# Kernel optimization log

Measured on AMD Instinct MI355X. Metric: run time of the kernel, lower is better.

Reference implementation:

```python
import jax, jax.numpy as jnp
import numpy as np

B, D, H = 65536, 32, 128


def setup_inputs() -> dict:
    key = jax.random.key(0)
    ks = jax.random.split(key, 6)
    return {
        "x": jax.random.normal(ks[0], (B, 1, D), dtype=jnp.float32),
        "W1": jax.random.normal(ks[1], (D, H), dtype=jnp.float32) * (1.0 / np.sqrt(D)),
        "b1": jax.random.normal(ks[2], (H,), dtype=jnp.float32) * 0.01,
        "W2": jax.random.normal(ks[3], (H, D), dtype=jnp.float32) * (1.0 / np.sqrt(H)),
        "b2": jax.random.normal(ks[4], (D,), dtype=jnp.float32) * 0.01,
        "theta_0": jnp.array([0.5], dtype=jnp.float32),
    }


def reference(x, W1, b1, W2, b2, theta_0):
    # x: (B, 1, D). Network u: D -> H -> D with tanh (transformation=none, no bounds).
    xf = x[:, 0, :]  # (B, D)

    def u_fn(xv):  # (D,) -> (D,)
        h = jnp.tanh(xv @ W1 + b1)
        return h @ W2 + b2

    # div u = trace of per-sample Jacobian, computed in ONE vectorized forward-mode
    # sweep (replaces the per-dimension torch.autograd.grad loop).
    div_u = jax.vmap(lambda xv: jnp.trace(jax.jacfwd(u_fn)(xv)))(xf)  # (B,)

    u_x = jax.vmap(u_fn)(xf)  # (B, D)
    grad_log_pi = -xf  # standard normal: grad log pi(x) = -x, shape (B, D)
    grad_log_pi_u = jnp.sum(grad_log_pi * u_x, axis=-1)  # (B,)  == (B,1,D)@(B,D,1) flattened

    out = (grad_log_pi_u + div_u + theta_0)[:, None]  # (B, 1)
    return out
```

## Files before the change

### kernel.cpp

```cpp
#include <hip/hip_runtime.h>


#define NROWS 65536
#define DD 32
#define HH 128
#define NTILE 25

typedef __attribute__((ext_vector_type(8))) short short8;
typedef __attribute__((ext_vector_type(4))) float f32x4;

static __device__ __forceinline__ unsigned short f2bf(float f) {
    unsigned u = __float_as_uint(f);
    u += 0x7fff + ((u >> 16) & 1);
    return (unsigned short)(u >> 16);
}
static __device__ __forceinline__ float bf2f(unsigned short h) {
    return __uint_as_float(((unsigned)h) << 16);
}

__global__ __launch_bounds__(512, 4) void stein_fused(
    const float* __restrict__ x, const float* __restrict__ W1,
    const float* __restrict__ b1, const float* __restrict__ W2,
    const float* __restrict__ b2, const float* __restrict__ theta,
    float* __restrict__ out) {
    __shared__ unsigned short lb[NTILE * 512];
    __shared__ float cs[HH];
    __shared__ float b1s[HH];

    const int tid = threadIdx.x;
    const int lane = tid & 63;
    const int wv = tid >> 6;
    const int quad = lane >> 4;
    const int cl = lane & 15;
    const int rowbase = blockIdx.x * 128 + wv * 16;

    const float* xr = x + (size_t)(rowbase + cl) * DD + quad * 8;
    const float4 x0 = *(const float4*)xr;
    const float4 x1 = *(const float4*)(xr + 4);

    if (tid < 256) {
        const int n = tid & 127;
        const int half = tid >> 7;
        const int t = n >> 4, cc = n & 15;
#pragma unroll
        for (int g = 0; g < 2; ++g) {
            const int kg = half * 2 + g;
            short8 hi, lo;
#pragma unroll
            for (int j = 0; j < 8; ++j) {
                const float w = W1[(kg * 8 + j) * HH + n];
                const unsigned short h = f2bf(w);
                hi[j] = (short)h;
                lo[j] = (short)f2bf(w - bf2f(h));
            }
            *(short8*)(lb + t * 512 + (kg * 16 + cc) * 8) = hi;
            *(short8*)(lb + (8 + t) * 512 + (kg * 16 + cc) * 8) = lo;
        }
    } else if (tid < 384) {
        const int n = tid - 256;
        const int t2 = 16 + (n >> 4), cc = n & 15;
        float row[32];
        const float4* wr = (const float4*)(W2 + n * DD);
#pragma unroll
        for (int q = 0; q < 8; ++q) {
            const float4 f = wr[q];
            row[4 * q + 0] = f.x;
            row[4 * q + 1] = f.y;
            row[4 * q + 2] = f.z;
            row[4 * q + 3] = f.w;
        }
        float acc = 0.f;
#pragma unroll
        for (int k = 0; k < 32; ++k) acc = fmaf(W1[k * HH + n], row[k], acc);
        cs[n] = acc;
#pragma unroll
        for (int g = 0; g < 4; ++g) {
            short8 v;
#pragma unroll
            for (int j = 0; j < 8; ++j) v[j] = (short)f2bf(row[g * 8 + j]);
            *(short8*)(lb + t2 * 512 + (g * 16 + cc) * 8) = v;
        }
    } else {
        const int u = tid - 384;
        if (u < 16) {
#pragma unroll
            for (int g = 0; g < 4; ++g) {
                short8 v;
#pragma unroll
                for (int j = 0; j < 8; ++j)
                    v[j] = (u == 0) ? (short)f2bf(b2[g * 8 + j]) : (short)0;
                *(short8*)(lb + 24 * 512 + (g * 16 + u) * 8) = v;
            }
        }
        b1s[u] = b1[u];
    }
    __syncthreads();

    const float xv[8] = {x0.x, x0.y, x0.z, x0.w, x1.x, x1.y, x1.z, x1.w};
    short8 aHi, aLo;
#pragma unroll
    for (int j = 0; j < 8; ++j) {
        const unsigned short h = f2bf(xv[j]);
        aHi[j] = (short)h;
        aLo[j] = (short)f2bf(xv[j] - bf2f(h));
    }

    const f32x4 zero = {0.f, 0.f, 0.f, 0.f};
    float sa[4] = {0.f, 0.f, 0.f, 0.f};

#pragma unroll
    for (int t = 0; t < 8; ++t) {
        const short8 bH = *(const short8*)(lb + t * 512 + lane * 8);
        const short8 bL = *(const short8*)(lb + (8 + t) * 512 + lane * 8);
        const short8 bW = *(const short8*)(lb + (16 + t) * 512 + lane * 8);
        f32x4 z = zero;
        z = __builtin_amdgcn_mfma_f32_16x16x32_bf16(aLo, bH, z, 0, 0, 0);
        z = __builtin_amdgcn_mfma_f32_16x16x32_bf16(aHi, bL, z, 0, 0, 0);
        z = __builtin_amdgcn_mfma_f32_16x16x32_bf16(aHi, bH, z, 0, 0, 0);
        const f32x4 v = __builtin_amdgcn_mfma_f32_16x16x32_bf16(aHi, bW, zero, 0, 0, 0);
        const float ck = cs[t * 16 + cl];
        const float bb = b1s[t * 16 + cl];
#pragma unroll
        for (int r = 0; r < 4; ++r) {
            const float zz = z[r] + bb;
            const float e = __expf(2.f * zz);
            const float h = fmaf(-2.f, __builtin_amdgcn_rcpf(e + 1.f), 1.f);
            sa[r] += ck - h * fmaf(h, ck, v[r]);
        }
    }
    {
        const short8 bW = *(const short8*)(lb + 24 * 512 + lane * 8);
        const f32x4 v = __builtin_amdgcn_mfma_f32_16x16x32_bf16(aHi, bW, zero, 0, 0, 0);
#pragma unroll
        for (int r = 0; r < 4; ++r) sa[r] -= v[r];
    }

#pragma unroll
    for (int r = 0; r < 4; ++r) {
#pragma unroll
        for (int m = 1; m < 16; m <<= 1) sa[r] += __shfl_xor(sa[r], m, 64);
    }

    if (cl == 0) {
        const float th = theta[0];
        float4 o;
        o.x = sa[0] + th;
        o.y = sa[1] + th;
        o.z = sa[2] + th;
        o.w = sa[3] + th;
        *(float4*)(out + rowbase + quad * 4) = o;
    }
}

extern "C" void kernel_launch(void* const* d_in, const int* in_sizes, int n_in,
                              void* d_out, int out_size, void* d_ws, size_t ws_size,
                              hipStream_t stream) {
    const float* x = (const float*)d_in[0];
    const float* W1 = (const float*)d_in[1];
    const float* b1 = (const float*)d_in[2];
    const float* W2 = (const float*)d_in[3];
    const float* b2 = (const float*)d_in[4];
    const float* theta = (const float*)d_in[5];
    float* out = (float*)d_out;

    stein_fused<<<NROWS / 128, 512, 0, stream>>>(x, W1, b1, W2, b2, theta, out);
}
```

Baseline: 72.03 us.

## Process two 16-row tiles per wave to amortize weight setup across more rows

Each wave now handles 32 rows instead of 16, reusing the same LDS B-fragments for two sets of MFMAs. The block count halves, so the per-block weight conversion prologue is amortized over twice as many rows. The c_k dot product moves to the previously idle threads 384-511, and the c and b1 values are packed into one float2 LDS array. Launch bounds drop to 2 blocks per SM, trading occupancy for more instruction-level parallelism and extra registers.

```diff
diff --git a/kernel.cpp b/kernel.cpp
--- a/kernel.cpp
+++ b/kernel.cpp
@@ -18,25 +18,27 @@
     return __uint_as_float(((unsigned)h) << 16);
 }
 
-__global__ __launch_bounds__(512, 4) void stein_fused(
+__global__ __launch_bounds__(512, 2) void stein_fused(
     const float* __restrict__ x, const float* __restrict__ W1,
     const float* __restrict__ b1, const float* __restrict__ W2,
     const float* __restrict__ b2, const float* __restrict__ theta,
     float* __restrict__ out) {
     __shared__ unsigned short lb[NTILE * 512];
-    __shared__ float cs[HH];
-    __shared__ float b1s[HH];
+    __shared__ float2 cb[HH];
 
     const int tid = threadIdx.x;
     const int lane = tid & 63;
     const int wv = tid >> 6;
     const int quad = lane >> 4;
     const int cl = lane & 15;
-    const int rowbase = blockIdx.x * 128 + wv * 16;
+    const int rowbase = blockIdx.x * 256 + wv * 32;
 
-    const float* xr = x + (size_t)(rowbase + cl) * DD + quad * 8;
-    const float4 x0 = *(const float4*)xr;
-    const float4 x1 = *(const float4*)(xr + 4);
+    const float* xr0 = x + (size_t)(rowbase + cl) * DD + quad * 8;
+    const float* xr1 = x + (size_t)(rowbase + 16 + cl) * DD + quad * 8;
+    const float4 x00 = *(const float4*)xr0;
+    const float4 x01 = *(const float4*)(xr0 + 4);
+    const float4 x10 = *(const float4*)xr1;
+    const float4 x11 = *(const float4*)(xr1 + 4);
 
     if (tid < 256) {
         const int n = tid & 127;
@@ -59,29 +61,32 @@
     } else if (tid < 384) {
         const int n = tid - 256;
         const int t2 = 16 + (n >> 4), cc = n & 15;
-        float row[32];
         const float4* wr = (const float4*)(W2 + n * DD);
 #pragma unroll
-        for (int q = 0; q < 8; ++q) {
-            const float4 f = wr[q];
-            row[4 * q + 0] = f.x;
-            row[4 * q + 1] = f.y;
-            row[4 * q + 2] = f.z;
-            row[4 * q + 3] = f.w;
-        }
-        float acc = 0.f;
-#pragma unroll
-        for (int k = 0; k < 32; ++k) acc = fmaf(W1[k * HH + n], row[k], acc);
-        cs[n] = acc;
-#pragma unroll
         for (int g = 0; g < 4; ++g) {
+            const float4 f0 = wr[2 * g];
+            const float4 f1 = wr[2 * g + 1];
             short8 v;
-#pragma unroll
-            for (int j = 0; j < 8; ++j) v[j] = (short)f2bf(row[g * 8 + j]);
+            v[0] = (short)f2bf(f0.x); v[1] = (short)f2bf(f0.y);
+            v[2] = (short)f2bf(f0.z); v[3] = (short)f2bf(f0.w);
+            v[4] = (short)f2bf(f1.x); v[5] = (short)f2bf(f1.y);
+            v[6] = (short)f2bf(f1.z); v[7] = (short)f2bf(f1.w);
             *(short8*)(lb + t2 * 512 + (g * 16 + cc) * 8) = v;
         }
     } else {
         const int u = tid - 384;
+        float row[DD];
+        const float4* wr = (const float4*)(W2 + u * DD);
+#pragma unroll
+        for (int q = 0; q < 8; ++q) {
+            const float4 f = wr[q];
+            row[4 * q + 0] = f.x; row[4 * q + 1] = f.y;
+            row[4 * q + 2] = f.z; row[4 * q + 3] = f.w;
+        }
+        float acc = 0.f;
+#pragma unroll
+        for (int k = 0; k < DD; ++k) acc = fmaf(W1[k * HH + u], row[k], acc);
+        cb[u] = make_float2(acc, b1[u]);
         if (u < 16) {
 #pragma unroll
             for (int g = 0; g < 4; ++g) {
@@ -92,63 +97,85 @@
                 *(short8*)(lb + 24 * 512 + (g * 16 + u) * 8) = v;
             }
         }
-        b1s[u] = b1[u];
     }
     __syncthreads();
 
-    const float xv[8] = {x0.x, x0.y, x0.z, x0.w, x1.x, x1.y, x1.z, x1.w};
-    short8 aHi, aLo;
+    short8 aHi0, aLo0, aHi1, aLo1;
+    {
+        const float xv0[8] = {x00.x, x00.y, x00.z, x00.w, x01.x, x01.y, x01.z, x01.w};
+        const float xv1[8] = {x10.x, x10.y, x10.z, x10.w, x11.x, x11.y, x11.z, x11.w};
 #pragma unroll
-    for (int j = 0; j < 8; ++j) {
-        const unsigned short h = f2bf(xv[j]);
-        aHi[j] = (short)h;
-        aLo[j] = (short)f2bf(xv[j] - bf2f(h));
+        for (int j = 0; j < 8; ++j) {
+            unsigned short h0 = f2bf(xv0[j]);
+            aHi0[j] = (short)h0;
+            aLo0[j] = (short)f2bf(xv0[j] - bf2f(h0));
+            unsigned short h1 = f2bf(xv1[j]);
+            aHi1[j] = (short)h1;
+            aLo1[j] = (short)f2bf(xv1[j] - bf2f(h1));
+        }
     }
 
     const f32x4 zero = {0.f, 0.f, 0.f, 0.f};
-    float sa[4] = {0.f, 0.f, 0.f, 0.f};
+    float sa0[4] = {0.f, 0.f, 0.f, 0.f};
+    float sa1[4] = {0.f, 0.f, 0.f, 0.f};
 
 #pragma unroll
     for (int t = 0; t < 8; ++t) {
         const short8 bH = *(const short8*)(lb + t * 512 + lane * 8);
         const short8 bL = *(const short8*)(lb + (8 + t) * 512 + lane * 8);
         const short8 bW = *(const short8*)(lb + (16 + t) * 512 + lane * 8);
-        f32x4 z = zero;
-        z = __builtin_amdgcn_mfma_f32_16x16x32_bf16(aLo, bH, z, 0, 0, 0);
-        z = __builtin_amdgcn_mfma_f32_16x16x32_bf16(aHi, bL, z, 0, 0, 0);
-        z = __builtin_amdgcn_mfma_f32_16x16x32_bf16(aHi, bH, z, 0, 0, 0);
-        const f32x4 v = __builtin_amdgcn_mfma_f32_16x16x32_bf16(aHi, bW, zero, 0, 0, 0);
-        const float ck = cs[t * 16 + cl];
-        const float bb = b1s[t * 16 + cl];
+        const float2 cbv = cb[t * 16 + cl];
+        f32x4 z0 = zero, z1 = zero;
+        z0 = __builtin_amdgcn_mfma_f32_16x16x32_bf16(aLo0, bH, z0, 0, 0, 0);
+        z1 = __builtin_amdgcn_mfma_f32_16x16x32_bf16(aLo1, bH, z1, 0, 0, 0);
+        z0 = __builtin_amdgcn_mfma_f32_16x16x32_bf16(aHi0, bL, z0, 0, 0, 0);
+        z1 = __builtin_amdgcn_mfma_f32_16x16x32_bf16(aHi1, bL, z1, 0, 0, 0);
+        z0 = __builtin_amdgcn_mfma_f32_16x16x32_bf16(aHi0, bH, z0, 0, 0, 0);
+        z1 = __builtin_amdgcn_mfma_f32_16x16x32_bf16(aHi1, bH, z1, 0, 0, 0);
+        const f32x4 v0 = __builtin_amdgcn_mfma_f32_16x16x32_bf16(aHi0, bW, zero, 0, 0, 0);
+        const f32x4 v1 = __builtin_amdgcn_mfma_f32_16x16x32_bf16(aHi1, bW, zero, 0, 0, 0);
 #pragma unroll
         for (int r = 0; r < 4; ++r) {
-            const float zz = z[r] + bb;
-            const float e = __expf(2.f * zz);
-            const float h = fmaf(-2.f, __builtin_amdgcn_rcpf(e + 1.f), 1.f);
-            sa[r] += ck - h * fmaf(h, ck, v[r]);
+            {
+                const float zz = z0[r] + cbv.y;
+                const float e = __expf(2.f * zz);
+                const float h = fmaf(-2.f, __builtin_amdgcn_rcpf(e + 1.f), 1.f);
+                sa0[r] += cbv.x - h * fmaf(h, cbv.x, v0[r]);
+            }
+            {
+                const float zz = z1[r] + cbv.y;
+                const float e = __expf(2.f * zz);
+                const float h = fmaf(-2.f, __builtin_amdgcn_rcpf(e + 1.f), 1.f);
+                sa1[r] += cbv.x - h * fmaf(h, cbv.x, v1[r]);
+            }
         }
     }
     {
         const short8 bW = *(const short8*)(lb + 24 * 512 + lane * 8);
-        const f32x4 v = __builtin_amdgcn_mfma_f32_16x16x32_bf16(aHi, bW, zero, 0, 0, 0);
+        const f32x4 v0 = __builtin_amdgcn_mfma_f32_16x16x32_bf16(aHi0, bW, zero, 0, 0, 0);
+        const f32x4 v1 = __builtin_amdgcn_mfma_f32_16x16x32_bf16(aHi1, bW, zero, 0, 0, 0);
 #pragma unroll
-        for (int r = 0; r < 4; ++r) sa[r] -= v[r];
+        for (int r = 0; r < 4; ++r) { sa0[r] -= v0[r]; sa1[r] -= v1[r]; }
     }
 
 #pragma unroll
     for (int r = 0; r < 4; ++r) {
 #pragma unroll
-        for (int m = 1; m < 16; m <<= 1) sa[r] += __shfl_xor(sa[r], m, 64);
+        for (int m = 1; m < 16; m <<= 1) {
+            sa0[r] += __shfl_xor(sa0[r], m, 64);
+            sa1[r] += __shfl_xor(sa1[r], m, 64);
+        }
     }
 
     if (cl == 0) {
         const float th = theta[0];
-        float4 o;
-        o.x = sa[0] + th;
-        o.y = sa[1] + th;
-        o.z = sa[2] + th;
-        o.w = sa[3] + th;
-        *(float4*)(out + rowbase + quad * 4) = o;
+        float4 o0, o1;
+        o0.x = sa0[0] + th; o0.y = sa0[1] + th;
+        o0.z = sa0[2] + th; o0.w = sa0[3] + th;
+        o1.x = sa1[0] + th; o1.y = sa1[1] + th;
+        o1.z = sa1[2] + th; o1.w = sa1[3] + th;
+        *(float4*)(out + rowbase + quad * 4) = o0;
+        *(float4*)(out + rowbase + 16 + quad * 4) = o1;
     }
 }
 
@@ -163,5 +190,5 @@
     const float* theta = (const float*)d_in[5];
     float* out = (float*)d_out;
 
-    stein_fused<<<NROWS / 128, 512, 0, stream>>>(x, W1, b1, W2, b2, theta, out);
+    stein_fused<<<NROWS / 256, 512, 0, stream>>>(x, W1, b1, W2, b2, theta, out);
 }
```

New measurement: 73.47 us. +2.0%, slower.

## Halve block size to 256 threads and pack cs/b1 into float2 LDS

Applied to the files above, without the earlier changes.

Blocks now process 64 rows with 256 threads, doubling the grid, and the weight-preparation work is redistributed over the two halves of the block. The c_k and b1 shared arrays are merged into one float2 array so each tile needs a single LDS load. The aim is better CU load balance and occupancy, at the cost of repeating the per-block W1/W2 conversion setup twice as often.

```diff
diff --git a/kernel.cpp b/kernel.cpp
--- a/kernel.cpp
+++ b/kernel.cpp
@@ -18,33 +18,30 @@
     return __uint_as_float(((unsigned)h) << 16);
 }
 
-__global__ __launch_bounds__(512, 4) void stein_fused(
+__global__ __launch_bounds__(256, 5) void stein_fused(
     const float* __restrict__ x, const float* __restrict__ W1,
     const float* __restrict__ b1, const float* __restrict__ W2,
     const float* __restrict__ b2, const float* __restrict__ theta,
     float* __restrict__ out) {
     __shared__ unsigned short lb[NTILE * 512];
-    __shared__ float cs[HH];
-    __shared__ float b1s[HH];
+    __shared__ float2 cb[HH];
 
     const int tid = threadIdx.x;
     const int lane = tid & 63;
     const int wv = tid >> 6;
     const int quad = lane >> 4;
     const int cl = lane & 15;
-    const int rowbase = blockIdx.x * 128 + wv * 16;
+    const int rowbase = blockIdx.x * 64 + wv * 16;
 
     const float* xr = x + (size_t)(rowbase + cl) * DD + quad * 8;
     const float4 x0 = *(const float4*)xr;
     const float4 x1 = *(const float4*)(xr + 4);
 
-    if (tid < 256) {
-        const int n = tid & 127;
-        const int half = tid >> 7;
+    if (tid < 128) {
+        const int n = tid;
         const int t = n >> 4, cc = n & 15;
 #pragma unroll
-        for (int g = 0; g < 2; ++g) {
-            const int kg = half * 2 + g;
+        for (int kg = 0; kg < 4; ++kg) {
             short8 hi, lo;
 #pragma unroll
             for (int j = 0; j < 8; ++j) {
@@ -56,23 +53,17 @@
             *(short8*)(lb + t * 512 + (kg * 16 + cc) * 8) = hi;
             *(short8*)(lb + (8 + t) * 512 + (kg * 16 + cc) * 8) = lo;
         }
-    } else if (tid < 384) {
-        const int n = tid - 256;
+    } else {
+        const int n = tid - 128;
         const int t2 = 16 + (n >> 4), cc = n & 15;
-        float row[32];
+        float row[DD];
         const float4* wr = (const float4*)(W2 + n * DD);
 #pragma unroll
         for (int q = 0; q < 8; ++q) {
             const float4 f = wr[q];
-            row[4 * q + 0] = f.x;
-            row[4 * q + 1] = f.y;
-            row[4 * q + 2] = f.z;
-            row[4 * q + 3] = f.w;
+            row[4 * q + 0] = f.x; row[4 * q + 1] = f.y;
+            row[4 * q + 2] = f.z; row[4 * q + 3] = f.w;
         }
-        float acc = 0.f;
-#pragma unroll
-        for (int k = 0; k < 32; ++k) acc = fmaf(W1[k * HH + n], row[k], acc);
-        cs[n] = acc;
 #pragma unroll
         for (int g = 0; g < 4; ++g) {
             short8 v;
@@ -80,19 +71,20 @@
             for (int j = 0; j < 8; ++j) v[j] = (short)f2bf(row[g * 8 + j]);
             *(short8*)(lb + t2 * 512 + (g * 16 + cc) * 8) = v;
         }
-    } else {
-        const int u = tid - 384;
-        if (u < 16) {
+        float acc = 0.f;
+#pragma unroll
+        for (int k = 0; k < DD; ++k) acc = fmaf(W1[k * HH + n], row[k], acc);
+        cb[n] = make_float2(acc, b1[n]);
+        if (n < 16) {
 #pragma unroll
             for (int g = 0; g < 4; ++g) {
                 short8 v;
 #pragma unroll
                 for (int j = 0; j < 8; ++j)
-                    v[j] = (u == 0) ? (short)f2bf(b2[g * 8 + j]) : (short)0;
-                *(short8*)(lb + 24 * 512 + (g * 16 + u) * 8) = v;
+                    v[j] = (n == 0) ? (short)f2bf(b2[g * 8 + j]) : (short)0;
+                *(short8*)(lb + 24 * 512 + (g * 16 + n) * 8) = v;
             }
         }
-        b1s[u] = b1[u];
     }
     __syncthreads();
 
@@ -113,19 +105,18 @@
         const short8 bH = *(const short8*)(lb + t * 512 + lane * 8);
         const short8 bL = *(const short8*)(lb + (8 + t) * 512 + lane * 8);
         const short8 bW = *(const short8*)(lb + (16 + t) * 512 + lane * 8);
+        const float2 cbv = cb[t * 16 + cl];
         f32x4 z = zero;
         z = __builtin_amdgcn_mfma_f32_16x16x32_bf16(aLo, bH, z, 0, 0, 0);
         z = __builtin_amdgcn_mfma_f32_16x16x32_bf16(aHi, bL, z, 0, 0, 0);
         z = __builtin_amdgcn_mfma_f32_16x16x32_bf16(aHi, bH, z, 0, 0, 0);
         const f32x4 v = __builtin_amdgcn_mfma_f32_16x16x32_bf16(aHi, bW, zero, 0, 0, 0);
-        const float ck = cs[t * 16 + cl];
-        const float bb = b1s[t * 16 + cl];
 #pragma unroll
         for (int r = 0; r < 4; ++r) {
-            const float zz = z[r] + bb;
+            const float zz = z[r] + cbv.y;
             const float e = __expf(2.f * zz);
             const float h = fmaf(-2.f, __builtin_amdgcn_rcpf(e + 1.f), 1.f);
-            sa[r] += ck - h * fmaf(h, ck, v[r]);
+            sa[r] += cbv.x - h * fmaf(h, cbv.x, v[r]);
         }
     }
     {
@@ -163,5 +154,5 @@
     const float* theta = (const float*)d_in[5];
     float* out = (float*)d_out;
 
-    stein_fused<<<NROWS / 128, 512, 0, stream>>>(x, W1, b1, W2, b2, theta, out);
+    stein_fused<<<NROWS / 64, 256, 0, stream>>>(x, W1, b1, W2, b2, theta, out);
 }
```

Measured after the change: 71.81 us. About the same (-0.3%).
